# Optimization experiments

Measured on AMD Instinct MI355X. Metric: run time of the kernel, lower is better.

## Reference

```python
import jax, jax.numpy as jnp
import numpy as np

B, T, E, WIN, OC, VOCAB = 256, 2048, 128, 5, 128, 50000


def setup_inputs() -> dict:
    key = jax.random.key(0)
    k1, k2, k3, k4, k5, k6 = jax.random.split(key, 6)
    return {
        "x": jax.random.randint(k1, (B, T), 0, VOCAB + 1, dtype=jnp.int32),
        "emb_table": jax.random.normal(k2, (VOCAB + 1, E), dtype=jnp.float32),
        "att_w": jax.random.normal(k3, (WIN, E), dtype=jnp.float32) * 0.05,
        "att_b": jax.random.normal(k4, (1,), dtype=jnp.float32),
        "cnn_w": jax.random.normal(k5, (OC, E), dtype=jnp.float32) * 0.05,
        "cnn_b": jax.random.normal(k6, (OC,), dtype=jnp.float32),
    }


def reference(x, emb_table, att_w, att_b, cnn_w, cnn_b):
    win = att_w.shape[0]
    pad = (win - 1) // 2
    embed = emb_table[x]                                   # [B, T, E]
    x_pad = jnp.pad(embed, ((0, 0), (pad, pad), (0, 0)))
    T_ = embed.shape[1]
    # Sliding-window dot product over full embed dim (the degenerate Conv2d)
    s = jnp.zeros(embed.shape[:2], dtype=embed.dtype)      # [B, T]
    for k in range(win):
        s = s + jnp.einsum('bte,e->bt', x_pad[:, k:k + T_, :], att_w[k])
    scores = jax.nn.sigmoid(s + att_b[0])                  # [B, T]
    gated = embed * scores[:, :, None]                     # [B, T, E]
    feat = jnp.tanh(jnp.einsum('bte,oe->bto', gated, cnn_w) + cnn_b)  # [B, T, OC]
    out = jnp.max(feat, axis=1)                            # [B, OC] (maxpool over seq)
    return out[:, :, None, None]                           # [B, OC, 1, 1]
```

## Files before the change

### kernel.cpp

```cpp
#include <hip/hip_runtime.h>
#include <hip/hip_bf16.h>
#include <math.h>

#define B_   256
#define T_   2048
#define E_   128
#define WIN_ 5
#define PAD_ 2
#define OC_  128
#define VOCAB_MAX 50000
#define VOCAB1 50001
#define TT   64
#define REAL_ROWS (TT + WIN_ - 1)
#define ROWS 80
#define ASTR 136
#define VROWS 64
#define BT   512

typedef __attribute__((ext_vector_type(8))) short short8;
typedef __attribute__((ext_vector_type(4))) float floatx4;
typedef __attribute__((ext_vector_type(4))) unsigned uintx4;

static __device__ __forceinline__ short f2bf(float f) {
    union { __hip_bfloat16 h; short s; } u;
    u.h = __float2bfloat16(f);
    return u.s;
}

__device__ __forceinline__ void atomicMaxFloat(float* addr, float v) {
    if (v >= 0.0f) atomicMax((int*)addr, __float_as_int(v));
    else           atomicMin((unsigned int*)addr, __float_as_uint(v));
}

__launch_bounds__(256, 4)
__global__ void build_tables(const float* __restrict__ emb,
                             const float* __restrict__ cnn_w,
                             const float* __restrict__ att_w,
                             short* __restrict__ D,
                             float* __restrict__ r,
                             float* __restrict__ out) {
    __shared__ short sh_a[VROWS * ASTR];

    const int tid  = threadIdx.x;
    const int lane = tid & 63;
    const int w    = tid >> 6;
    const int l15  = lane & 15;
    const int quad = lane >> 4;
    const int v0   = blockIdx.x * VROWS;

    if (blockIdx.x < (B_ * OC_) / 256)
        out[blockIdx.x * 256 + tid] = -INFINITY;

    #pragma unroll
    for (int t = 0; t < 8; t++) {
        int i   = t * 256 + tid;
        int row = i >> 5, c4 = i & 31;
        int vr  = v0 + row; if (vr > VOCAB_MAX) vr = VOCAB_MAX;
        float4 v = *(const float4*)(emb + (size_t)vr * E_ + c4 * 4);
        short4 o; o.x = f2bf(v.x); o.y = f2bf(v.y); o.z = f2bf(v.z); o.w = f2bf(v.w);
        *(short4*)(&sh_a[row * ASTR + c4 * 4]) = o;
    }

    short8 Bf[2][4];
    #pragma unroll
    for (int j = 0; j < 2; j++)
        #pragma unroll
        for (int ks = 0; ks < 4; ks++) {
            const float4* p = (const float4*)(cnn_w + (size_t)(w * 32 + j * 16 + l15) * E_ + ks * 32 + quad * 8);
            float4 p0 = p[0], p1 = p[1];
            Bf[j][ks] = (short8){ f2bf(p0.x), f2bf(p0.y), f2bf(p0.z), f2bf(p0.w),
                                  f2bf(p1.x), f2bf(p1.y), f2bf(p1.z), f2bf(p1.w) };
        }

    short8 Ba[4];
    #pragma unroll
    for (int ks = 0; ks < 4; ks++) {
        short8 v = (short8){0,0,0,0,0,0,0,0};
        if (l15 < WIN_) {
            const float4* p = (const float4*)(att_w + (size_t)l15 * E_ + ks * 32 + quad * 8);
            float4 p0 = p[0], p1 = p[1];
            v = (short8){ f2bf(p0.x), f2bf(p0.y), f2bf(p0.z), f2bf(p0.w),
                          f2bf(p1.x), f2bf(p1.y), f2bf(p1.z), f2bf(p1.w) };
        }
        Ba[ks] = v;
    }
    __syncthreads();

    #pragma unroll
    for (int mt = 0; mt < 4; mt++) {
        short8 a[4];
        #pragma unroll
        for (int ks = 0; ks < 4; ks++)
            a[ks] = *(const short8*)(&sh_a[(mt * 16 + l15) * ASTR + ks * 32 + quad * 8]);
        #pragma unroll
        for (int j = 0; j < 2; j++) {
            floatx4 acc = (floatx4){0.f, 0.f, 0.f, 0.f};
            #pragma unroll
            for (int ks = 0; ks < 4; ks++)
                acc = __builtin_amdgcn_mfma_f32_16x16x32_bf16(a[ks], Bf[j][ks], acc, 0, 0, 0);
            #pragma unroll
            for (int rr = 0; rr < 4; rr++) {
                int v = v0 + mt * 16 + quad * 4 + rr;
                if (v <= VOCAB_MAX)
                    D[(size_t)v * E_ + w * 32 + j * 16 + l15] = f2bf(acc[rr]);
            }
        }
    }

    {
        short8 a[4];
        #pragma unroll
        for (int ks = 0; ks < 4; ks++)
            a[ks] = *(const short8*)(&sh_a[(w * 16 + l15) * ASTR + ks * 32 + quad * 8]);
        floatx4 acc = (floatx4){0.f, 0.f, 0.f, 0.f};
        #pragma unroll
        for (int ks = 0; ks < 4; ks++)
            acc = __builtin_amdgcn_mfma_f32_16x16x32_bf16(a[ks], Ba[ks], acc, 0, 0, 0);
        if (l15 < 8) {
            #pragma unroll
            for (int rr = 0; rr < 4; rr++) {
                int v = v0 + w * 16 + quad * 4 + rr;
                if (v <= VOCAB_MAX) r[(size_t)v * 8 + l15] = acc[rr];
            }
        }
    }
}

__launch_bounds__(256, 6)
__global__ void score_max(const int* __restrict__ x,
                          const short* __restrict__ D,
                          const float* __restrict__ r,
                          const float* __restrict__ att_b_p,
                          const float* __restrict__ cnn_b,
                          float* __restrict__ out) {
    __shared__ int   sh_x[BT + 4];
    __shared__ float sh_rt[WIN_][BT + 8];
    __shared__ float sh_sc[BT];
    __shared__ float sh_red[4][128];

    const int tid  = threadIdx.x;
    const int lane = tid & 63;
    const int w    = tid >> 6;
    const int b    = blockIdx.y;
    const int t0   = blockIdx.x * BT;
    const int l15  = lane & 15;
    const int grp  = lane >> 4;

    for (int i = tid; i < BT + 4; i += 256) {
        int t = t0 + i - PAD_;
        sh_x[i] = (t >= 0 && t < T_) ? x[b * T_ + t] : -1;
    }
    __syncthreads();

    for (int i = tid; i < BT + 4; i += 256) {
        int v = sh_x[i];
        float4 r03 = make_float4(0.f, 0.f, 0.f, 0.f);
        float  r4  = 0.f;
        if (v >= 0) {
            r03 = *(const float4*)(r + (size_t)v * 8);
            r4  = r[(size_t)v * 8 + 4];
        }
        sh_rt[0][i] = r03.x; sh_rt[1][i] = r03.y; sh_rt[2][i] = r03.z;
        sh_rt[3][i] = r03.w; sh_rt[4][i] = r4;
    }
    __syncthreads();

    {
        const float attb = att_b_p[0];
        #pragma unroll
        for (int rep = 0; rep < 2; rep++) {
            int j = rep * 256 + tid;
            float s = attb;
            #pragma unroll
            for (int k = 0; k < WIN_; k++) s += sh_rt[k][j + k];
            sh_sc[j] = 1.0f / (1.0f + __expf(-s));
        }
    }
    __syncthreads();

    float mm[8];
    #pragma unroll
    for (int c = 0; c < 8; c++) mm[c] = -INFINITY;

    const int base_t = w * 128;
    for (int batch = 0; batch < 4; batch++) {
        uintx4 u[8];
        float  sc8[8];
        const int start = base_t + batch * 32;
        #pragma unroll
        for (int j = 0; j < 8; j++) {
            int tok = start + j * 4 + grp;
            int v   = sh_x[tok + PAD_];
            sc8[j]  = sh_sc[tok];
            u[j]    = *(const uintx4*)(D + (size_t)v * E_ + l15 * 8);
        }
        #pragma unroll
        for (int j = 0; j < 8; j++) {
            #pragma unroll
            for (int q = 0; q < 4; q++) {
                float lo = __uint_as_float(u[j][q] << 16);
                float hi = __uint_as_float(u[j][q] & 0xFFFF0000u);
                mm[q * 2]     = fmaxf(mm[q * 2],     sc8[j] * lo);
                mm[q * 2 + 1] = fmaxf(mm[q * 2 + 1], sc8[j] * hi);
            }
        }
    }
    #pragma unroll
    for (int c = 0; c < 8; c++) {
        mm[c] = fmaxf(mm[c], __shfl_xor(mm[c], 16));
        mm[c] = fmaxf(mm[c], __shfl_xor(mm[c], 32));
    }
    if (lane < 16) {
        #pragma unroll
        for (int c = 0; c < 8; c++) sh_red[w][l15 * 8 + c] = mm[c];
    }
    __syncthreads();
    if (tid < 128) {
        float m = fmaxf(fmaxf(sh_red[0][tid], sh_red[1][tid]),
                        fmaxf(sh_red[2][tid], sh_red[3][tid]));
        atomicMaxFloat(&out[b * OC_ + tid], tanhf(m + cnn_b[tid]));
    }
}

__global__ void prep_small(const float* __restrict__ cnn_w, const float* __restrict__ att_w,
                           short* __restrict__ wsw, short* __restrict__ wsatt) {
    int i = blockIdx.x * 256 + threadIdx.x;
    if (i < OC_ * E_)  wsw[i]   = f2bf(cnn_w[i]);
    if (i < WIN_ * E_) wsatt[i] = f2bf(att_w[i]);
}

__launch_bounds__(256, 4)
__global__ void fallback_main(const int* __restrict__ x,
                              const float* __restrict__ emb,
                              const float* __restrict__ att_b_p,
                              const short* __restrict__ wsw,
                              const short* __restrict__ wsatt,
                              const float* __restrict__ cnn_b,
                              float* __restrict__ out) {
    __shared__ short sh_a[ROWS * ASTR];
    __shared__ short sh_att[16 * ASTR];
    __shared__ float sh_r[ROWS * 8];
    __shared__ float sh_score[TT];
    __shared__ int   sh_idx[8 * ROWS];

    const int tid  = threadIdx.x;
    const int lane = tid & 63;
    const int w    = tid >> 6;
    const int b    = blockIdx.y;
    const int t0   = blockIdx.x * (8 * TT);
    const int l15  = lane & 15;
    const int quad = lane >> 4;
    const int rbase = tid >> 4;
    const int c     = tid & 15;

    for (int i = tid; i < 8 * ROWS; i += 256) {
        int tile = i / ROWS, row = i - tile * ROWS;
        int t = t0 + tile * TT + row - PAD_;
        sh_idx[i] = (row < REAL_ROWS && t >= 0 && t < T_) ? x[b * T_ + t] : -1;
    }
    {
        int o = tid >> 4, cc = tid & 15;
        short8 v = (short8){0,0,0,0,0,0,0,0};
        if (o < WIN_) v = *(const short8*)(wsatt + o * E_ + cc * 8);
        *(short8*)(&sh_att[o * ASTR + cc * 8]) = v;
    }
    short8 Bf[2][4];
    #pragma unroll
    for (int j = 0; j < 2; j++)
        #pragma unroll
        for (int ks = 0; ks < 4; ks++)
            Bf[j][ks] = *(const short8*)(wsw + (size_t)(w * 32 + j * 16 + l15) * E_ + ks * 32 + quad * 8);
    __syncthreads();

    short8 g[5];
    #pragma unroll
    for (int k = 0; k < 5; k++) {
        int idx = sh_idx[rbase + 16 * k];
        short8 v = (short8){0,0,0,0,0,0,0,0};
        if (idx >= 0) {
            const float4* p = (const float4*)(emb + (size_t)idx * E_ + c * 8);
            float4 p0 = p[0], p1 = p[1];
            v = (short8){ f2bf(p0.x), f2bf(p0.y), f2bf(p0.z), f2bf(p0.w),
                          f2bf(p1.x), f2bf(p1.y), f2bf(p1.z), f2bf(p1.w) };
        }
        g[k] = v;
    }
    #pragma unroll
    for (int k = 0; k < 5; k++)
        *(short8*)(&sh_a[(rbase + 16 * k) * ASTR + c * 8]) = g[k];
    __syncthreads();

    const float attb = att_b_p[0];
    float mm[2] = { -INFINITY, -INFINITY };

    for (int it = 0; it < 8; it++) {
        for (int mt = w; mt < 5; mt += 4) {
            floatx4 acc = (floatx4){0.f, 0.f, 0.f, 0.f};
            #pragma unroll
            for (int ks = 0; ks < 4; ks++) {
                short8 a  = *(const short8*)(&sh_a[(mt * 16 + l15) * ASTR + ks * 32 + quad * 8]);
                short8 bs = *(const short8*)(&sh_att[l15 * ASTR + ks * 32 + quad * 8]);
                acc = __builtin_amdgcn_mfma_f32_16x16x32_bf16(a, bs, acc, 0, 0, 0);
            }
            if (l15 < 8) {
                #pragma unroll
                for (int r = 0; r < 4; r++)
                    sh_r[(mt * 16 + quad * 4 + r) * 8 + l15] = acc[r];
            }
        }
        __syncthreads();

        if (it + 1 < 8) {
            const int* idxp = &sh_idx[(it + 1) * ROWS];
            #pragma unroll
            for (int k = 0; k < 5; k++) {
                int idx = idxp[rbase + 16 * k];
                short8 v = (short8){0,0,0,0,0,0,0,0};
                if (idx >= 0) {
                    const float4* p = (const float4*)(emb + (size_t)idx * E_ + c * 8);
                    float4 p0 = p[0], p1 = p[1];
                    v = (short8){ f2bf(p0.x), f2bf(p0.y), f2bf(p0.z), f2bf(p0.w),
                                  f2bf(p1.x), f2bf(p1.y), f2bf(p1.z), f2bf(p1.w) };
                }
                g[k] = v;
            }
        }

        if (tid < TT) {
            float s = attb;
            #pragma unroll
            for (int k = 0; k < WIN_; k++) s += sh_r[(tid + k) * 8 + k];
            sh_score[tid] = 1.0f / (1.0f + __expf(-s));
        }

        floatx4 acc[4][2];
        #pragma unroll
        for (int i = 0; i < 4; i++)
            #pragma unroll
            for (int j = 0; j < 2; j++) acc[i][j] = (floatx4){0.f, 0.f, 0.f, 0.f};
        #pragma unroll
        for (int ks = 0; ks < 4; ks++) {
            int ko = ks * 32 + quad * 8;
            #pragma unroll
            for (int i = 0; i < 4; i++) {
                short8 ai = *(const short8*)(&sh_a[(PAD_ + i * 16 + l15) * ASTR + ko]);
                acc[i][0] = __builtin_amdgcn_mfma_f32_16x16x32_bf16(ai, Bf[0][ks], acc[i][0], 0, 0, 0);
                acc[i][1] = __builtin_amdgcn_mfma_f32_16x16x32_bf16(ai, Bf[1][ks], acc[i][1], 0, 0, 0);
            }
        }
        __syncthreads();

        #pragma unroll
        for (int i = 0; i < 4; i++) {
            #pragma unroll
            for (int r = 0; r < 4; r++) {
                float sc = sh_score[i * 16 + quad * 4 + r];
                mm[0] = fmaxf(mm[0], sc * acc[i][0][r]);
                mm[1] = fmaxf(mm[1], sc * acc[i][1][r]);
            }
        }

        if (it + 1 < 8) {
            #pragma unroll
            for (int k = 0; k < 5; k++)
                *(short8*)(&sh_a[(rbase + 16 * k) * ASTR + c * 8]) = g[k];
            __syncthreads();
        }
    }

    #pragma unroll
    for (int j = 0; j < 2; j++) {
        float m = mm[j];
        m = fmaxf(m, __shfl_xor(m, 16));
        m = fmaxf(m, __shfl_xor(m, 32));
        if (lane < 16) {
            int o = w * 32 + j * 16 + lane;
            atomicMaxFloat(&out[b * OC_ + o], tanhf(m + cnn_b[o]));
        }
    }
}

extern "C" void kernel_launch(void* const* d_in, const int* in_sizes, int n_in,
                              void* d_out, int out_size, void* d_ws, size_t ws_size,
                              hipStream_t stream) {
    const int*   x     = (const int*)d_in[0];
    const float* emb   = (const float*)d_in[1];
    const float* att_w = (const float*)d_in[2];
    const float* att_b = (const float*)d_in[3];
    const float* cnn_w = (const float*)d_in[4];
    const float* cnn_b = (const float*)d_in[5];
    float* out = (float*)d_out;

    const size_t d_elems = (size_t)VOCAB1 * E_;
    const size_t r_elems = (size_t)VOCAB1 * 8;
    const size_t need = d_elems * 2 + r_elems * 4 + 64;

    if (ws_size >= need) {
        short* Dt = (short*)d_ws;
        float* rt = (float*)(Dt + d_elems);
        build_tables<<<(VOCAB1 + VROWS - 1) / VROWS, 256, 0, stream>>>(emb, cnn_w, att_w, Dt, rt, out);
        dim3 grid(T_ / BT, B_);
        score_max<<<grid, 256, 0, stream>>>(x, Dt, rt, att_b, cnn_b, out);
    } else {
        hipMemsetAsync(d_out, 0xFF, (size_t)B_ * OC_ * sizeof(float), stream);
        short* ws_w   = (short*)d_ws;
        short* ws_att = ws_w + OC_ * E_;
        prep_small<<<16, 256, 0, stream>>>(cnn_w, att_w, ws_w, ws_att);
        dim3 grid(T_ / (8 * TT), B_);
        fallback_main<<<grid, 256, 0, stream>>>(x, emb, att_b, ws_w, ws_att, cnn_b, out);
    }
}
```

Measured before the change: 112.0 us.

## Double-buffer table gathers in score_max and vectorize MFMA output stores

The score_max loop now prefetches the next batch of gathered D rows into a second register buffer while computing on the current batch, to hide gather latency. To make room for the extra registers, launch bounds occupancy drops from 6 to 5. In the precompute kernel, the MFMA operands are swapped so each lane holds contiguous output elements, and the D and r writes become packed vector stores instead of scattered scalar stores. The cost is higher register pressure and lower occupancy in score_max.

```diff
diff --git a/kernel.cpp b/kernel.cpp
--- a/kernel.cpp
+++ b/kernel.cpp
@@ -92,17 +92,18 @@
         #pragma unroll
         for (int ks = 0; ks < 4; ks++)
             a[ks] = *(const short8*)(&sh_a[(mt * 16 + l15) * ASTR + ks * 32 + quad * 8]);
+        const int v = v0 + mt * 16 + l15;
         #pragma unroll
         for (int j = 0; j < 2; j++) {
             floatx4 acc = (floatx4){0.f, 0.f, 0.f, 0.f};
             #pragma unroll
             for (int ks = 0; ks < 4; ks++)
-                acc = __builtin_amdgcn_mfma_f32_16x16x32_bf16(a[ks], Bf[j][ks], acc, 0, 0, 0);
-            #pragma unroll
-            for (int rr = 0; rr < 4; rr++) {
-                int v = v0 + mt * 16 + quad * 4 + rr;
-                if (v <= VOCAB_MAX)
-                    D[(size_t)v * E_ + w * 32 + j * 16 + l15] = f2bf(acc[rr]);
+                acc = __builtin_amdgcn_mfma_f32_16x16x32_bf16(Bf[j][ks], a[ks], acc, 0, 0, 0);
+            if (v <= VOCAB_MAX) {
+                short4 pk;
+                pk.x = f2bf(acc[0]); pk.y = f2bf(acc[1]);
+                pk.z = f2bf(acc[2]); pk.w = f2bf(acc[3]);
+                *(short4*)(D + (size_t)v * E_ + w * 32 + j * 16 + quad * 4) = pk;
             }
         }
     }
@@ -115,18 +116,14 @@
         floatx4 acc = (floatx4){0.f, 0.f, 0.f, 0.f};
         #pragma unroll
         for (int ks = 0; ks < 4; ks++)
-            acc = __builtin_amdgcn_mfma_f32_16x16x32_bf16(a[ks], Ba[ks], acc, 0, 0, 0);
-        if (l15 < 8) {
-            #pragma unroll
-            for (int rr = 0; rr < 4; rr++) {
-                int v = v0 + w * 16 + quad * 4 + rr;
-                if (v <= VOCAB_MAX) r[(size_t)v * 8 + l15] = acc[rr];
-            }
-        }
-    }
-}
-
-__launch_bounds__(256, 6)
+            acc = __builtin_amdgcn_mfma_f32_16x16x32_bf16(Ba[ks], a[ks], acc, 0, 0, 0);
+        const int v = v0 + w * 16 + l15;
+        if (quad < 2 && v <= VOCAB_MAX)
+            *(floatx4*)(r + (size_t)v * 8 + quad * 4) = acc;
+    }
+}
+
+__launch_bounds__(256, 5)
 __global__ void score_max(const int* __restrict__ x,
                           const short* __restrict__ D,
                           const float* __restrict__ r,
@@ -183,28 +180,44 @@
     for (int c = 0; c < 8; c++) mm[c] = -INFINITY;
 
     const int base_t = w * 128;
+    uintx4 ua[8], ub[8];
+
+    #pragma unroll
+    for (int j = 0; j < 8; j++) {
+        int tok = base_t + j * 4 + grp;
+        int v   = sh_x[tok + PAD_];
+        ua[j]   = *(const uintx4*)(D + (size_t)v * E_ + l15 * 8);
+    }
+
+    #pragma unroll
     for (int batch = 0; batch < 4; batch++) {
-        uintx4 u[8];
-        float  sc8[8];
-        const int start = base_t + batch * 32;
+        if (batch + 1 < 4) {
+            const int start = base_t + (batch + 1) * 32;
+            #pragma unroll
+            for (int j = 0; j < 8; j++) {
+                int tok = start + j * 4 + grp;
+                int v   = sh_x[tok + PAD_];
+                ub[j]   = *(const uintx4*)(D + (size_t)v * E_ + l15 * 8);
+            }
+        }
+        const int cstart = base_t + batch * 32;
         #pragma unroll
         for (int j = 0; j < 8; j++) {
-            int tok = start + j * 4 + grp;
-            int v   = sh_x[tok + PAD_];
-            sc8[j]  = sh_sc[tok];
-            u[j]    = *(const uintx4*)(D + (size_t)v * E_ + l15 * 8);
-        }
-        #pragma unroll
-        for (int j = 0; j < 8; j++) {
+            float sc = sh_sc[cstart + j * 4 + grp];
             #pragma unroll
             for (int q = 0; q < 4; q++) {
-                float lo = __uint_as_float(u[j][q] << 16);
-                float hi = __uint_as_float(u[j][q] & 0xFFFF0000u);
-                mm[q * 2]     = fmaxf(mm[q * 2],     sc8[j] * lo);
-                mm[q * 2 + 1] = fmaxf(mm[q * 2 + 1], sc8[j] * hi);
-            }
-        }
-    }
+                float lo = __uint_as_float(ua[j][q] << 16);
+                float hi = __uint_as_float(ua[j][q] & 0xFFFF0000u);
+                mm[q * 2]     = fmaxf(mm[q * 2],     sc * lo);
+                mm[q * 2 + 1] = fmaxf(mm[q * 2 + 1], sc * hi);
+            }
+        }
+        if (batch + 1 < 4) {
+            #pragma unroll
+            for (int j = 0; j < 8; j++) ua[j] = ub[j];
+        }
+    }
+
     #pragma unroll
     for (int c = 0; c < 8; c++) {
         mm[c] = fmaxf(mm[c], __shfl_xor(mm[c], 16));
```

Result: no change. 112.3 us (+0.3%).
